# Optimization experiments

Hardware: AMD Instinct MI355X
Metric: run time of the kernel (lower is better)

The kernel has to match this reference:

```python
import jax, jax.numpy as jnp
import numpy as np
from jax import lax

FP = 64   # frame side
DP = 28   # digit template side
CP = FP - DP + 1  # 37, valid correlation output side


def setup_inputs() -> dict:
    key = jax.random.key(0)
    ks = jax.random.split(key, 6)
    B, T, S, H = 128, 16, 10, 256
    frames = jax.random.normal(ks[0], (B, T, FP, FP), dtype=jnp.float32)
    digit_images = jax.random.uniform(ks[1], (S, B, DP, DP), dtype=jnp.float32)
    W1 = jax.random.normal(ks[2], (CP * CP, H), dtype=jnp.float32) * (1.0 / np.sqrt(CP * CP))
    b1 = jnp.zeros((H,), dtype=jnp.float32)
    W2 = jax.random.normal(ks[3], (H, 2), dtype=jnp.float32) * (1.0 / np.sqrt(H))
    b2 = jnp.zeros((2,), dtype=jnp.float32)
    where_std = jnp.ones((2,), dtype=jnp.float32) * 0.1
    return {"frames": frames, "digit_images": digit_images, "S": S,
            "W1": W1, "b1": b1, "W2": W2, "b2": b2, "where_std": where_std}


def reference(frames, digit_images, S, W1, b1, W2, b2, where_std):
    B, T = frames.shape[0], frames.shape[1]
    # torch: conv2d(frames.transpose(0,1), digit_images.view(S*B,DP,DP).unsqueeze(1), groups=B)
    # lhs: (T, B, FP, FP) treated as batch=T, channels=B; rhs: (S*B, 1, DP, DP)
    lhs = jnp.transpose(frames, (1, 0, 2, 3))              # (T, B, FP, FP)
    rhs = digit_images.reshape(S * B, 1, DP, DP)           # (S*B, 1, DP, DP)
    convolved = lax.conv_general_dilated(
        lhs, rhs, window_strides=(1, 1), padding='VALID',
        feature_group_count=B,
        dimension_numbers=('NCHW', 'OIHW', 'NCHW'))        # (T, S*B, CP, CP)
    convolved = convolved.reshape(T, S, B, CP * CP)
    hidden = jnp.tanh(convolved @ W1 + b1)                 # (T, S, B, H)
    q_mean = jnp.tanh(hidden @ W2 + b2)                    # (T, S, B, 2)
    q_mean = jnp.transpose(q_mean, (1, 2, 0, 3))           # (S, B, T, 2)
    eps = jax.random.normal(jax.random.key(1), q_mean.shape, dtype=q_mean.dtype)
    z_where = q_mean + where_std * eps                     # Normal(q_mean, std).sample()
    return q_mean, z_where
```

## Files before the change

kernel.cpp:

```cpp
#include <hip/hip_runtime.h>
#include <stdint.h>

#define CROWB 2816
#define NOUT 40960
#define DGB 32832
#define DGSTR 920

typedef _Float16 f16x8 __attribute__((ext_vector_type(8)));
typedef float f32x4 __attribute__((ext_vector_type(4)));

#define TF_ROT(x, r) (((x) << (r)) | ((x) >> (32 - (r))))
#define TF_ROUND(r) { x0 += x1; x1 = TF_ROT(x1, (r)); x1 ^= x0; }

__device__ __forceinline__ float erfinv_f(float x) {
  float w = -log1pf(-x * x);
  float p;
  if (w < 5.0f) {
    w -= 2.5f;
    p = 2.81022636e-08f;
    p = fmaf(p, w, 3.43273939e-07f);
    p = fmaf(p, w, -3.5233877e-06f);
    p = fmaf(p, w, -4.39150654e-06f);
    p = fmaf(p, w, 0.00021858087f);
    p = fmaf(p, w, -0.00125372503f);
    p = fmaf(p, w, -0.00417768164f);
    p = fmaf(p, w, 0.246640727f);
    p = fmaf(p, w, 1.50140941f);
  } else {
    w = sqrtf(w) - 3.0f;
    p = -0.000200214257f;
    p = fmaf(p, w, 0.000100950558f);
    p = fmaf(p, w, 0.00134934322f);
    p = fmaf(p, w, -0.00367342844f);
    p = fmaf(p, w, 0.00573950773f);
    p = fmaf(p, w, -0.0076224613f);
    p = fmaf(p, w, 0.00943887047f);
    p = fmaf(p, w, 1.00167406f);
    p = fmaf(p, w, 2.83297682f);
  }
  return p * x;
}

__device__ __forceinline__ float gauss_eps(int p) {
  const unsigned ks0 = 0u, ks1 = 1u, ks2 = 0x1BD11BDBu;
  unsigned x0 = 0u + ks0;
  unsigned x1 = (unsigned)p + ks1;
  TF_ROUND(13) TF_ROUND(15) TF_ROUND(26) TF_ROUND(6)
  x0 += ks1; x1 += ks2 + 1u;
  TF_ROUND(17) TF_ROUND(29) TF_ROUND(16) TF_ROUND(24)
  x0 += ks2; x1 += ks0 + 2u;
  TF_ROUND(13) TF_ROUND(15) TF_ROUND(26) TF_ROUND(6)
  x0 += ks0; x1 += ks1 + 3u;
  TF_ROUND(17) TF_ROUND(29) TF_ROUND(16) TF_ROUND(24)
  x0 += ks1; x1 += ks2 + 4u;
  TF_ROUND(13) TF_ROUND(15) TF_ROUND(26) TF_ROUND(6)
  x0 += ks2; x1 += ks0 + 5u;
  unsigned bits = x0 ^ x1;
  unsigned fb = (bits >> 9) | 0x3f800000u;
  float f = __uint_as_float(fb) - 1.0f;
  const float lo = -0.99999994f;
  float u = f * 2.0f + lo;
  u = fmaxf(lo, u);
  return 1.41421356f * erfinv_f(u);
}

__device__ __forceinline__ float fast_tanh(float x) {
  float e = __expf(2.0f * x);
  return 1.0f - 2.0f * __builtin_amdgcn_rcpf(e + 1.0f);
}

__device__ __forceinline__ uint32_t packh2(float lo, float hi) {
  union { _Float16 h[2]; uint32_t u; } c;
  c.h[0] = (_Float16)lo; c.h[1] = (_Float16)hi;
  return c.u;
}

__global__ void prep_w1t(const float* __restrict__ W1, uint8_t* __restrict__ w1t) {
  int k = blockIdx.x;
  int h = threadIdx.x;
  float v = (k < 1369) ? W1[(size_t)k * 256 + h] : 0.0f;
  *(_Float16*)(w1t + (size_t)h * CROWB + (size_t)k * 2) = (_Float16)v;
}

__global__ __launch_bounds__(256, 2) void conv_mfma(
    const float* __restrict__ frames, const float* __restrict__ digits,
    uint8_t* __restrict__ conv_out)
{
  __shared__ __align__(16) uint8_t smem[62272];
  const int g = blockIdx.x >> 4, t = blockIdx.x & 15;
  const int tid = threadIdx.x;
  const int lane = tid & 63, w = tid >> 6;
  const int l15 = lane & 15, lg = lane >> 4;
  const int jo = lg * 8;

  {
    const float* fbase = frames + ((size_t)(g * 16 + t)) * 4096;
    float h[20];
    const float4* f4 = (const float4*)(fbase + tid * 16);
    #pragma unroll
    for (int a = 0; a < 4; ++a) {
      float4 v = f4[a];
      h[4*a] = v.x; h[4*a+1] = v.y; h[4*a+2] = v.z; h[4*a+3] = v.w;
    }
    float t0 = __shfl_down(h[0], 1), t1 = __shfl_down(h[1], 1),
          t2 = __shfl_down(h[2], 1), t3 = __shfl_down(h[3], 1);
    if (lane == 63) {
      int bidx = tid * 16 + 16;
      t0 = (bidx + 0 < 4096) ? fbase[bidx + 0] : 0.0f;
      t1 = (bidx + 1 < 4096) ? fbase[bidx + 1] : 0.0f;
      t2 = (bidx + 2 < 4096) ? fbase[bidx + 2] : 0.0f;
      t3 = (bidx + 3 < 4096) ? fbase[bidx + 3] : 0.0f;
    }
    h[16] = t0; h[17] = t1; h[18] = t2; h[19] = t3;
    #pragma unroll
    for (int c = 0; c < 8; ++c) {
      int cc = (c + tid) & 7;
      int le = 2 * cc;
      uint4 v;
      v.x = packh2(h[le],   h[le+1]);
      v.y = packh2(h[le+2], h[le+3]);
      v.z = packh2(h[le+1], h[le+2]);
      v.w = packh2(h[le+3], h[le+4]);
      *(uint4*)(smem + 128 * tid + 16 * cc) = v;
    }
    if (tid < 16) *(uint32_t*)(smem + 32768 + tid * 4) = 0u;
  }
  {
    uint32_t* dz = (uint32_t*)(smem + DGB);
    for (int q = tid; q < 7360; q += 256) dz[q] = 0u;
  }
  __syncthreads();
  {
    const float* dsrc = digits + (size_t)g * 7840;
    for (int idx = tid; idx < 7840; idx += 256) {
      int s = idx / 784; int r = idx - s * 784;
      int i = r / 28;    int j = r - i * 28;
      *(_Float16*)(smem + DGB + (size_t)(s * DGSTR + i * 32 + j) * 2) = (_Float16)dsrc[idx];
    }
  }
  __syncthreads();

  uint32_t abase[22];
  #pragma unroll
  for (int j2 = 0; j2 < 22; ++j2) {
    int tile = w + 4 * j2;
    int p = tile * 16 + l15;
    int py = p / 37, px = p - py * 37;
    abase[j2] = (uint32_t)(py * 64 + px + jo) * 8u;
  }

  f32x4 acc[22];
  #pragma unroll
  for (int j2 = 0; j2 < 22; ++j2) acc[j2] = (f32x4){0.f, 0.f, 0.f, 0.f};

  for (int i = 0; i < 28; ++i) {
    f16x8 bfrag = *(const f16x8*)(smem + DGB + (size_t)(l15 * DGSTR + i * 32 + jo) * 2);
    #pragma unroll
    for (int j2 = 0; j2 < 22; ++j2) {
      const uint8_t* ap = smem + abase[j2] + i * 512;
      union { uint2 u2[2]; f16x8 v; } A;
      A.u2[0] = *(const uint2*)(ap);
      A.u2[1] = *(const uint2*)(ap + 32);
      acc[j2] = __builtin_amdgcn_mfma_f32_16x16x32_f16(A.v, bfrag, acc[j2], 0, 0, 0);
    }
  }

  if (l15 < 10) {
    size_t rb = ((size_t)t * 1280 + 10 * g + l15) * (size_t)CROWB;
    #pragma unroll
    for (int j2 = 0; j2 < 22; ++j2) {
      int p0 = (w + 4 * j2) * 16 + lg * 4;
      #pragma unroll
      for (int r = 0; r < 4; ++r) {
        int p = p0 + r;
        if (p < 1369)
          *(_Float16*)(conv_out + rb + (size_t)p * 2) = (_Float16)acc[j2][r];
      }
    }
  }
}

__global__ __launch_bounds__(256) void mlp_mfma(
    const uint8_t* __restrict__ conv_out, const uint8_t* __restrict__ w1t,
    const float* __restrict__ b1, const float* __restrict__ W2,
    const float* __restrict__ b2, const float* __restrict__ wstd,
    float* __restrict__ out)
{
  __shared__ __align__(16) uint8_t smem[43008];
  const int tid = threadIdx.x;
  const int lane = tid & 63, w = tid >> 6;
  const int l15 = lane & 15, lg = lane >> 4;
  const int m0 = blockIdx.x * 64;

  f32x4 acc[4][4];
  #pragma unroll
  for (int mt = 0; mt < 4; ++mt)
    #pragma unroll
    for (int nj = 0; nj < 4; ++nj) acc[mt][nj] = (f32x4){0.f, 0.f, 0.f, 0.f};

  for (int k0 = 0; k0 < 1408; k0 += 64) {
    __syncthreads();
    #pragma unroll
    for (int it = 0; it < 2; ++it) {
      int q = tid + 256 * it; int R = q >> 3, c16 = q & 7;
      uint4 v = *(const uint4*)(conv_out + (size_t)(m0 + R) * CROWB + (size_t)k0 * 2 + c16 * 16);
      *(uint4*)(smem + R * 128 + ((c16 * 16) ^ ((R & 7) << 4))) = v;
    }
    #pragma unroll
    for (int it = 0; it < 8; ++it) {
      int q = tid + 256 * it; int h = q >> 3, c16 = q & 7;
      uint4 v = *(const uint4*)(w1t + (size_t)h * CROWB + (size_t)k0 * 2 + c16 * 16);
      *(uint4*)(smem + 8192 + h * 128 + ((c16 * 16) ^ ((h & 7) << 4))) = v;
    }
    __syncthreads();
    #pragma unroll
    for (int q = 0; q < 2; ++q) {
      f16x8 bf[4];
      #pragma unroll
      for (int nj = 0; nj < 4; ++nj) {
        int h = (w * 4 + nj) * 16 + l15;
        bf[nj] = *(const f16x8*)(smem + 8192 + h * 128 + ((q * 64 + lg * 16) ^ ((h & 7) << 4)));
      }
      #pragma unroll
      for (int mt = 0; mt < 4; ++mt) {
        int R = mt * 16 + l15;
        union { uint4 u; f16x8 v; } A;
        A.u = *(const uint4*)(smem + R * 128 + ((q * 64 + lg * 16) ^ ((R & 7) << 4)));
        #pragma unroll
        for (int nj = 0; nj < 4; ++nj)
          acc[mt][nj] = __builtin_amdgcn_mfma_f32_16x16x32_f16(A.v, bf[nj], acc[mt][nj], 0, 0, 0);
      }
    }
  }

  float qp[4][4][2];
  #pragma unroll
  for (int mt = 0; mt < 4; ++mt)
    #pragma unroll
    for (int r = 0; r < 4; ++r) { qp[mt][r][0] = 0.f; qp[mt][r][1] = 0.f; }

  #pragma unroll
  for (int nj = 0; nj < 4; ++nj) {
    int h = (w * 4 + nj) * 16 + l15;
    float bb = b1[h];
    float w20 = W2[2 * h], w21 = W2[2 * h + 1];
    #pragma unroll
    for (int mt = 0; mt < 4; ++mt)
      #pragma unroll
      for (int r = 0; r < 4; ++r) {
        float hid = fast_tanh(acc[mt][nj][r] + bb);
        qp[mt][r][0] = fmaf(hid, w20, qp[mt][r][0]);
        qp[mt][r][1] = fmaf(hid, w21, qp[mt][r][1]);
      }
  }
  #pragma unroll
  for (int off = 1; off <= 8; off <<= 1) {
    #pragma unroll
    for (int mt = 0; mt < 4; ++mt)
      #pragma unroll
      for (int r = 0; r < 4; ++r) {
        qp[mt][r][0] += __shfl_xor(qp[mt][r][0], off);
        qp[mt][r][1] += __shfl_xor(qp[mt][r][1], off);
      }
  }
  float* qb = (float*)(smem + 40960);
  if (l15 == 0) {
    #pragma unroll
    for (int mt = 0; mt < 4; ++mt)
      #pragma unroll
      for (int r = 0; r < 4; ++r) {
        int row = mt * 16 + lg * 4 + r;
        qb[(w * 64 + row) * 2 + 0] = qp[mt][r][0];
        qb[(w * 64 + row) * 2 + 1] = qp[mt][r][1];
      }
  }
  __syncthreads();
  if (tid < 128) {
    int row = tid >> 1, c = tid & 1;
    float sum = qb[row * 2 + c] + qb[(64 + row) * 2 + c] +
                qb[(128 + row) * 2 + c] + qb[(192 + row) * 2 + c];
    float q = fast_tanh(sum + b2[c]);
    int m = m0 + row;
    int tt = m / 1280;
    int o = m - tt * 1280;
    int base = (o * 16 + tt) * 2;
    out[base + c] = q;
    out[NOUT + base + c] = q + wstd[c] * gauss_eps(base + c);
  }
}

extern "C" void kernel_launch(void* const* d_in, const int* in_sizes, int n_in,
                              void* d_out, int out_size, void* d_ws, size_t ws_size,
                              hipStream_t stream) {
  const float* frames = (const float*)d_in[0];
  const float* digits = (const float*)d_in[1];
  const float* W1   = (const float*)d_in[3];
  const float* b1   = (const float*)d_in[4];
  const float* W2   = (const float*)d_in[5];
  const float* b2   = (const float*)d_in[6];
  const float* wstd = (const float*)d_in[7];
  uint8_t* conv_ws = (uint8_t*)d_ws;
  uint8_t* w1t     = conv_ws + (size_t)20480 * CROWB;
  float* out = (float*)d_out;

  prep_w1t<<<dim3(1408), dim3(256), 0, stream>>>(W1, w1t);
  conv_mfma<<<dim3(2048), dim3(256), 0, stream>>>(frames, digits, conv_ws);
  mlp_mfma<<<dim3(320), dim3(256), 0, stream>>>(conv_ws, w1t, b1, W2, b2, wstd, out);
}
```

Baseline: 268.3 us.

## Compact digit smem, raise conv occupancy, prefetch MLP tiles, vectorize W1 transpose

```diff
diff --git a/kernel.cpp b/kernel.cpp
--- a/kernel.cpp
+++ b/kernel.cpp
@@ -4,7 +4,6 @@
 #define CROWB 2816
 #define NOUT 40960
 #define DGB 32832
-#define DGSTR 920
 
 typedef _Float16 f16x8 __attribute__((ext_vector_type(8)));
 typedef float f32x4 __attribute__((ext_vector_type(4)));
@@ -75,18 +74,29 @@
   return c.u;
 }
 
-__global__ void prep_w1t(const float* __restrict__ W1, uint8_t* __restrict__ w1t) {
-  int k = blockIdx.x;
-  int h = threadIdx.x;
-  float v = (k < 1369) ? W1[(size_t)k * 256 + h] : 0.0f;
-  *(_Float16*)(w1t + (size_t)h * CROWB + (size_t)k * 2) = (_Float16)v;
-}
-
-__global__ __launch_bounds__(256, 2) void conv_mfma(
+__global__ __launch_bounds__(256) void prep_w1t(const float* __restrict__ W1,
+                                                uint8_t* __restrict__ w1t) {
+  int k0 = blockIdx.x * 16;
+  int tid = threadIdx.x;
+  float v[16];
+  #pragma unroll
+  for (int r = 0; r < 16; ++r) {
+    int k = k0 + r;
+    v[r] = (k < 1369) ? W1[(size_t)k * 256 + tid] : 0.0f;
+  }
+  uint32_t o[8];
+  #pragma unroll
+  for (int a = 0; a < 8; ++a) o[a] = packh2(v[2*a], v[2*a+1]);
+  uint8_t* dst = w1t + (size_t)tid * CROWB + (size_t)k0 * 2;
+  *(uint4*)(dst)      = make_uint4(o[0], o[1], o[2], o[3]);
+  *(uint4*)(dst + 16) = make_uint4(o[4], o[5], o[6], o[7]);
+}
+
+__global__ __launch_bounds__(256, 3) void conv_mfma(
     const float* __restrict__ frames, const float* __restrict__ digits,
     uint8_t* __restrict__ conv_out)
 {
-  __shared__ __align__(16) uint8_t smem[62272];
+  __shared__ __align__(16) uint8_t smem[52992];
   const int g = blockIdx.x >> 4, t = blockIdx.x & 15;
   const int tid = threadIdx.x;
   const int lane = tid & 63, w = tid >> 6;
@@ -127,7 +137,7 @@
   }
   {
     uint32_t* dz = (uint32_t*)(smem + DGB);
-    for (int q = tid; q < 7360; q += 256) dz[q] = 0u;
+    for (int q = tid; q < 5040; q += 256) dz[q] = 0u;
   }
   __syncthreads();
   {
@@ -135,7 +145,7 @@
     for (int idx = tid; idx < 7840; idx += 256) {
       int s = idx / 784; int r = idx - s * 784;
       int i = r / 28;    int j = r - i * 28;
-      *(_Float16*)(smem + DGB + (size_t)(s * DGSTR + i * 32 + j) * 2) = (_Float16)dsrc[idx];
+      *(_Float16*)(smem + DGB + (size_t)(i * 360 + s * 36 + j) * 2) = (_Float16)dsrc[idx];
     }
   }
   __syncthreads();
@@ -148,13 +158,15 @@
     int py = p / 37, px = p - py * 37;
     abase[j2] = (uint32_t)(py * 64 + px + jo) * 8u;
   }
+  const int s2 = (l15 < 10) ? l15 : 0;
+  const uint32_t bbase = DGB + (uint32_t)(s2 * 36 + jo) * 2u;
 
   f32x4 acc[22];
   #pragma unroll
   for (int j2 = 0; j2 < 22; ++j2) acc[j2] = (f32x4){0.f, 0.f, 0.f, 0.f};
 
   for (int i = 0; i < 28; ++i) {
-    f16x8 bfrag = *(const f16x8*)(smem + DGB + (size_t)(l15 * DGSTR + i * 32 + jo) * 2);
+    f16x8 bfrag = *(const f16x8*)(smem + bbase + i * 720);
     #pragma unroll
     for (int j2 = 0; j2 < 22; ++j2) {
       const uint8_t* ap = smem + abase[j2] + i * 512;
@@ -186,43 +198,66 @@
     const float* __restrict__ b2, const float* __restrict__ wstd,
     float* __restrict__ out)
 {
-  __shared__ __align__(16) uint8_t smem[43008];
+  __shared__ __align__(16) uint8_t smem[45568];
   const int tid = threadIdx.x;
   const int lane = tid & 63, w = tid >> 6;
   const int l15 = lane & 15, lg = lane >> 4;
-  const int m0 = blockIdx.x * 64;
-
-  f32x4 acc[4][4];
-  #pragma unroll
-  for (int mt = 0; mt < 4; ++mt)
+  const int m0 = blockIdx.x * 80;
+
+  int aR[3], ac16[3]; bool av[3];
+  #pragma unroll
+  for (int it = 0; it < 3; ++it) {
+    int q = tid + 256 * it;
+    av[it] = (q < 640); aR[it] = q >> 3; ac16[it] = q & 7;
+  }
+  int bR[8], bc16[8];
+  #pragma unroll
+  for (int it = 0; it < 8; ++it) {
+    int q = tid + 256 * it;
+    bR[it] = q >> 3; bc16[it] = q & 7;
+  }
+
+  f32x4 acc[5][4];
+  #pragma unroll
+  for (int mt = 0; mt < 5; ++mt)
     #pragma unroll
     for (int nj = 0; nj < 4; ++nj) acc[mt][nj] = (f32x4){0.f, 0.f, 0.f, 0.f};
+
+  uint4 ra[3], rb[8];
+  #pragma unroll
+  for (int it = 0; it < 3; ++it)
+    if (av[it]) ra[it] = *(const uint4*)(conv_out + (size_t)(m0 + aR[it]) * CROWB + ac16[it] * 16);
+  #pragma unroll
+  for (int it = 0; it < 8; ++it)
+    rb[it] = *(const uint4*)(w1t + (size_t)bR[it] * CROWB + bc16[it] * 16);
 
   for (int k0 = 0; k0 < 1408; k0 += 64) {
     __syncthreads();
     #pragma unroll
-    for (int it = 0; it < 2; ++it) {
-      int q = tid + 256 * it; int R = q >> 3, c16 = q & 7;
-      uint4 v = *(const uint4*)(conv_out + (size_t)(m0 + R) * CROWB + (size_t)k0 * 2 + c16 * 16);
-      *(uint4*)(smem + R * 128 + ((c16 * 16) ^ ((R & 7) << 4))) = v;
-    }
-    #pragma unroll
-    for (int it = 0; it < 8; ++it) {
-      int q = tid + 256 * it; int h = q >> 3, c16 = q & 7;
-      uint4 v = *(const uint4*)(w1t + (size_t)h * CROWB + (size_t)k0 * 2 + c16 * 16);
-      *(uint4*)(smem + 8192 + h * 128 + ((c16 * 16) ^ ((h & 7) << 4))) = v;
-    }
+    for (int it = 0; it < 3; ++it)
+      if (av[it]) *(uint4*)(smem + aR[it] * 128 + ((ac16[it] * 16) ^ ((aR[it] & 7) << 4))) = ra[it];
+    #pragma unroll
+    for (int it = 0; it < 8; ++it)
+      *(uint4*)(smem + 10240 + bR[it] * 128 + ((bc16[it] * 16) ^ ((bR[it] & 7) << 4))) = rb[it];
     __syncthreads();
+    if (k0 + 64 < 1408) {
+      #pragma unroll
+      for (int it = 0; it < 3; ++it)
+        if (av[it]) ra[it] = *(const uint4*)(conv_out + (size_t)(m0 + aR[it]) * CROWB + (size_t)(k0 + 64) * 2 + ac16[it] * 16);
+      #pragma unroll
+      for (int it = 0; it < 8; ++it)
+        rb[it] = *(const uint4*)(w1t + (size_t)bR[it] * CROWB + (size_t)(k0 + 64) * 2 + bc16[it] * 16);
+    }
     #pragma unroll
     for (int q = 0; q < 2; ++q) {
       f16x8 bf[4];
       #pragma unroll
       for (int nj = 0; nj < 4; ++nj) {
         int h = (w * 4 + nj) * 16 + l15;
-        bf[nj] = *(const f16x8*)(smem + 8192 + h * 128 + ((q * 64 + lg * 16) ^ ((h & 7) << 4)));
-      }
-      #pragma unroll
-      for (int mt = 0; mt < 4; ++mt) {
+        bf[nj] = *(const f16x8*)(smem + 10240 + h * 128 + ((q * 64 + lg * 16) ^ ((h & 7) << 4)));
+      }
+      #pragma unroll
+      for (int mt = 0; mt < 5; ++mt) {
         int R = mt * 16 + l15;
         union { uint4 u; f16x8 v; } A;
         A.u = *(const uint4*)(smem + R * 128 + ((q * 64 + lg * 16) ^ ((R & 7) << 4)));
@@ -233,9 +268,9 @@
     }
   }
 
-  float qp[4][4][2];
-  #pragma unroll
-  for (int mt = 0; mt < 4; ++mt)
+  float qp[5][4][2];
+  #pragma unroll
+  for (int mt = 0; mt < 5; ++mt)
     #pragma unroll
     for (int r = 0; r < 4; ++r) { qp[mt][r][0] = 0.f; qp[mt][r][1] = 0.f; }
 
@@ -245,7 +280,7 @@
     float bb = b1[h];
     float w20 = W2[2 * h], w21 = W2[2 * h + 1];
     #pragma unroll
-    for (int mt = 0; mt < 4; ++mt)
+    for (int mt = 0; mt < 5; ++mt)
       #pragma unroll
       for (int r = 0; r < 4; ++r) {
         float hid = fast_tanh(acc[mt][nj][r] + bb);
@@ -256,29 +291,29 @@
   #pragma unroll
   for (int off = 1; off <= 8; off <<= 1) {
     #pragma unroll
-    for (int mt = 0; mt < 4; ++mt)
+    for (int mt = 0; mt < 5; ++mt)
       #pragma unroll
       for (int r = 0; r < 4; ++r) {
         qp[mt][r][0] += __shfl_xor(qp[mt][r][0], off);
         qp[mt][r][1] += __shfl_xor(qp[mt][r][1], off);
       }
   }
-  float* qb = (float*)(smem + 40960);
+  float* qb = (float*)(smem + 43008);
   if (l15 == 0) {
     #pragma unroll
-    for (int mt = 0; mt < 4; ++mt)
+    for (int mt = 0; mt < 5; ++mt)
       #pragma unroll
       for (int r = 0; r < 4; ++r) {
         int row = mt * 16 + lg * 4 + r;
-        qb[(w * 64 + row) * 2 + 0] = qp[mt][r][0];
-        qb[(w * 64 + row) * 2 + 1] = qp[mt][r][1];
+        qb[(w * 80 + row) * 2 + 0] = qp[mt][r][0];
+        qb[(w * 80 + row) * 2 + 1] = qp[mt][r][1];
       }
   }
   __syncthreads();
-  if (tid < 128) {
+  if (tid < 160) {
     int row = tid >> 1, c = tid & 1;
-    float sum = qb[row * 2 + c] + qb[(64 + row) * 2 + c] +
-                qb[(128 + row) * 2 + c] + qb[(192 + row) * 2 + c];
+    float sum = qb[row * 2 + c] + qb[(80 + row) * 2 + c] +
+                qb[(160 + row) * 2 + c] + qb[(240 + row) * 2 + c];
     float q = fast_tanh(sum + b2[c]);
     int m = m0 + row;
     int tt = m / 1280;
@@ -303,7 +338,7 @@
   uint8_t* w1t     = conv_ws + (size_t)20480 * CROWB;
   float* out = (float*)d_out;
 
-  prep_w1t<<<dim3(1408), dim3(256), 0, stream>>>(W1, w1t);
+  prep_w1t<<<dim3(88), dim3(256), 0, stream>>>(W1, w1t);
   conv_mfma<<<dim3(2048), dim3(256), 0, stream>>>(frames, digits, conv_ws);
-  mlp_mfma<<<dim3(320), dim3(256), 0, stream>>>(conv_ws, w1t, b1, W2, b2, wstd, out);
-}
+  mlp_mfma<<<dim3(256), dim3(256), 0, stream>>>(conv_ws, w1t, b1, W2, b2, wstd, out);
+}
```

Result: slower. 315.3 us (+17.5%).
